# Optimization experiments

Hardware: AMD Instinct MI355X
Metric: run time of the kernel (lower is better)

Reference implementation:

```python
import jax, jax.numpy as jnp
import numpy as np

N_NODES = 20000
N_EDGES = 640000
HIDDEN = 128


def setup_inputs() -> dict:
    key = jax.random.key(0)
    k1, k2, k3, k4 = jax.random.split(key, 4)
    scale = 1.0 / np.sqrt(HIDDEN)
    features = jax.random.normal(k1, (N_NODES, HIDDEN), dtype=jnp.float32)
    edge_index = jax.random.randint(k2, (2, N_EDGES), 0, N_NODES, dtype=jnp.int64)
    W_l = jax.random.normal(k3, (HIDDEN, HIDDEN), dtype=jnp.float32) * scale
    b_l = jnp.zeros((HIDDEN,), dtype=jnp.float32)
    W_r = jax.random.normal(k4, (HIDDEN, HIDDEN), dtype=jnp.float32) * scale
    return {"features": features, "edge_index": edge_index, "W_l": W_l, "b_l": b_l, "W_r": W_r}


def reference(features, edge_index, W_l, b_l, W_r):
    # PyG SAGEConv with mean aggregation:
    #   out_i = lin_l(mean_{j : (j->i) in E} x_j) + lin_r(x_i)
    # edge_index[0] = source nodes, edge_index[1] = target nodes.
    n = features.shape[0]
    src = edge_index[0]
    dst = edge_index[1]
    msg = features[src]  # [E, d] gather
    summed = jax.ops.segment_sum(msg, dst, num_segments=n)  # [N, d] scatter-add
    cnt = jax.ops.segment_sum(jnp.ones(src.shape[0], dtype=features.dtype), dst, num_segments=n)
    agg = summed / jnp.maximum(cnt, 1.0)[:, None]  # mean; isolated nodes -> 0
    return agg @ W_l.T + b_l + features @ W_r.T
```

## Files before the change

kernel.cpp:

```cpp
#include <hip/hip_runtime.h>

#define N_NODES 20000
#define N_EDGES 640000
#define HIDDEN  128
#define CAP     96
#define DEG_PAD 16

typedef unsigned short bf16_t;
typedef __attribute__((ext_vector_type(8))) short short8;
typedef __attribute__((ext_vector_type(8))) unsigned short ushort8_t;
typedef __attribute__((ext_vector_type(4))) float floatx4;

__device__ __forceinline__ bf16_t f2bf(float f) {
    union { float f; unsigned int i; } v; v.f = f;
    unsigned int x = v.i + 0x7FFFu + ((v.i >> 16) & 1u);
    return (bf16_t)(x >> 16);
}
__device__ __forceinline__ float bflo(unsigned u) {
    union { unsigned i; float f; } v; v.i = u << 16; return v.f;
}
__device__ __forceinline__ float bfhi(unsigned u) {
    union { unsigned i; float f; } v; v.i = u & 0xFFFF0000u; return v.f;
}

__global__ __launch_bounds__(256) void prep_fill_kernel(
        const float* __restrict__ feat,
        const float* __restrict__ Wl,
        const float* __restrict__ Wr,
        const int* __restrict__ eidx,
        bf16_t* __restrict__ feat_bf,
        bf16_t* __restrict__ Bp,
        int* __restrict__ deg,
        unsigned short* __restrict__ bucket) {
    int t = blockIdx.x * 256 + threadIdx.x;
    float4 v = ((const float4*)feat)[t];
    ushort4 o = { f2bf(v.x), f2bf(v.y), f2bf(v.z), f2bf(v.w) };
    ((ushort4*)feat_bf)[t] = o;
    int src = eidx[t];
    int dst = eidx[N_EDGES + t];
    int pos = atomicAdd(&deg[dst * DEG_PAD], 1);
    if (pos < CAP) bucket[dst * CAP + pos] = (unsigned short)src;
    if (t < 2 * HIDDEN * HIDDEN) {
        int j    = t & 7;
        int lane = (t >> 3) & 63;
        int nt   = (t >> 9) & 7;
        int kt   = t >> 12;
        int n = nt * 16 + (lane & 15);
        int k = kt * 32 + (lane >> 4) * 8 + j;
        float w = (k < HIDDEN) ? Wl[n * HIDDEN + k] : Wr[n * HIDDEN + (k - HIDDEN)];
        Bp[t] = f2bf(w);
    }
}

__global__ __launch_bounds__(256) void agg_kernel(
        const bf16_t* __restrict__ feat_bf,
        const int* __restrict__ deg,
        const unsigned short* __restrict__ bucket,
        bf16_t* __restrict__ agg) {
    int wid  = (blockIdx.x * 256 + threadIdx.x) >> 6;
    int lane = threadIdx.x & 63;
    if (wid >= N_NODES) return;
    int d_true = deg[wid * DEG_PAD];
    int d = min(d_true, CAP);
    const unsigned short* row = bucket + wid * CAP;
    const unsigned* y = (const unsigned*)feat_bf;
    float ax0=0,ay0=0, ax1=0,ay1=0, ax2=0,ay2=0, ax3=0,ay3=0;
    int i = 0;
    for (; i + 16 <= d; i += 16) {
        ushort8_t s0 = *(const ushort8_t*)(row + i);
        ushort8_t s1 = *(const ushort8_t*)(row + i + 8);
        unsigned u0 = y[(int)s0[0] * 64 + lane];
        unsigned u1 = y[(int)s0[1] * 64 + lane];
        unsigned u2 = y[(int)s0[2] * 64 + lane];
        unsigned u3 = y[(int)s0[3] * 64 + lane];
        unsigned u4 = y[(int)s0[4] * 64 + lane];
        unsigned u5 = y[(int)s0[5] * 64 + lane];
        unsigned u6 = y[(int)s0[6] * 64 + lane];
        unsigned u7 = y[(int)s0[7] * 64 + lane];
        unsigned w0 = y[(int)s1[0] * 64 + lane];
        unsigned w1 = y[(int)s1[1] * 64 + lane];
        unsigned w2 = y[(int)s1[2] * 64 + lane];
        unsigned w3 = y[(int)s1[3] * 64 + lane];
        unsigned w4 = y[(int)s1[4] * 64 + lane];
        unsigned w5 = y[(int)s1[5] * 64 + lane];
        unsigned w6 = y[(int)s1[6] * 64 + lane];
        unsigned w7 = y[(int)s1[7] * 64 + lane];
        ax0 += bflo(u0); ay0 += bfhi(u0);
        ax1 += bflo(u1); ay1 += bfhi(u1);
        ax2 += bflo(u2); ay2 += bfhi(u2);
        ax3 += bflo(u3); ay3 += bfhi(u3);
        ax0 += bflo(u4); ay0 += bfhi(u4);
        ax1 += bflo(u5); ay1 += bfhi(u5);
        ax2 += bflo(u6); ay2 += bfhi(u6);
        ax3 += bflo(u7); ay3 += bfhi(u7);
        ax0 += bflo(w0); ay0 += bfhi(w0);
        ax1 += bflo(w1); ay1 += bfhi(w1);
        ax2 += bflo(w2); ay2 += bfhi(w2);
        ax3 += bflo(w3); ay3 += bfhi(w3);
        ax0 += bflo(w4); ay0 += bfhi(w4);
        ax1 += bflo(w5); ay1 += bfhi(w5);
        ax2 += bflo(w6); ay2 += bfhi(w6);
        ax3 += bflo(w7); ay3 += bfhi(w7);
    }
    for (; i + 8 <= d; i += 8) {
        ushort8_t s = *(const ushort8_t*)(row + i);
        unsigned u0 = y[(int)s[0] * 64 + lane];
        unsigned u1 = y[(int)s[1] * 64 + lane];
        unsigned u2 = y[(int)s[2] * 64 + lane];
        unsigned u3 = y[(int)s[3] * 64 + lane];
        unsigned u4 = y[(int)s[4] * 64 + lane];
        unsigned u5 = y[(int)s[5] * 64 + lane];
        unsigned u6 = y[(int)s[6] * 64 + lane];
        unsigned u7 = y[(int)s[7] * 64 + lane];
        ax0 += bflo(u0); ay0 += bfhi(u0);
        ax1 += bflo(u1); ay1 += bfhi(u1);
        ax2 += bflo(u2); ay2 += bfhi(u2);
        ax3 += bflo(u3); ay3 += bfhi(u3);
        ax0 += bflo(u4); ay0 += bfhi(u4);
        ax1 += bflo(u5); ay1 += bfhi(u5);
        ax2 += bflo(u6); ay2 += bfhi(u6);
        ax3 += bflo(u7); ay3 += bfhi(u7);
    }
    for (; i < d; ++i) {
        unsigned u = y[(int)row[i] * 64 + lane];
        ax0 += bflo(u); ay0 += bfhi(u);
    }
    float inv = 1.0f / fmaxf((float)d_true, 1.0f);
    float sx = (ax0 + ax1 + ax2 + ax3) * inv;
    float sy = (ay0 + ay1 + ay2 + ay3) * inv;
    unsigned pk = (unsigned)f2bf(sx) | ((unsigned)f2bf(sy) << 16);
    ((unsigned*)agg)[wid * 64 + lane] = pk;
}

__global__ __launch_bounds__(256) void gemm_out_kernel(
        const bf16_t* __restrict__ agg,
        const bf16_t* __restrict__ feat_bf,
        const bf16_t* __restrict__ Bp,
        const float* __restrict__ bl,
        float* __restrict__ out) {
    int wid = blockIdx.x * 4 + (threadIdx.x >> 6);
    if (wid >= N_NODES / 16) return;
    int lane = threadIdx.x & 63;
    int m    = lane & 15;
    int quad = lane >> 4;
    int row0 = wid * 16;

    floatx4 acc[8];
    floatx4 zf = {0.f, 0.f, 0.f, 0.f};
#pragma unroll
    for (int nt = 0; nt < 8; ++nt) acc[nt] = zf;

    const short8* bp = (const short8*)Bp;
#pragma unroll
    for (int kt = 0; kt < 8; ++kt) {
        const bf16_t* abase = (kt < 4)
            ? (agg     + (size_t)(row0 + m) * HIDDEN + kt * 32 + quad * 8)
            : (feat_bf + (size_t)(row0 + m) * HIDDEN + (kt - 4) * 32 + quad * 8);
        short8 afrag = *(const short8*)abase;
#pragma unroll
        for (int nt = 0; nt < 8; ++nt) {
            short8 bfrag = bp[(kt * 8 + nt) * 64 + lane];
            acc[nt] = __builtin_amdgcn_mfma_f32_16x16x32_bf16(afrag, bfrag, acc[nt], 0, 0, 0);
        }
    }
    int col = lane & 15;
#pragma unroll
    for (int nt = 0; nt < 8; ++nt) {
        float b = bl[nt * 16 + col];
#pragma unroll
        for (int r = 0; r < 4; ++r) {
            int row = row0 + quad * 4 + r;
            out[(size_t)row * HIDDEN + nt * 16 + col] = acc[nt][r] + b;
        }
    }
}

extern "C" void kernel_launch(void* const* d_in, const int* in_sizes, int n_in,
                              void* d_out, int out_size, void* d_ws, size_t ws_size,
                              hipStream_t stream) {
    const float* feat = (const float*)d_in[0];
    const int*   eidx = (const int*)d_in[1];
    const float* Wl   = (const float*)d_in[2];
    const float* bl   = (const float*)d_in[3];
    const float* Wr   = (const float*)d_in[4];
    float* out = (float*)d_out;

    int*            deg     = (int*)d_ws;
    unsigned short* bucket  = (unsigned short*)(deg + N_NODES * DEG_PAD);
    bf16_t*         Bp      = (bf16_t*)(bucket + (size_t)N_NODES * CAP);
    bf16_t*         feat_bf = Bp + 2 * HIDDEN * HIDDEN;
    bf16_t*         agg     = feat_bf + (size_t)N_NODES * HIDDEN;

    hipMemsetAsync(deg, 0, (size_t)N_NODES * DEG_PAD * sizeof(int), stream);

    prep_fill_kernel<<<N_EDGES / 256, 256, 0, stream>>>(
        feat, Wl, Wr, eidx, feat_bf, Bp, deg, bucket);
    agg_kernel<<<(N_NODES * 64) / 256, 256, 0, stream>>>(feat_bf, deg, bucket, agg);
    gemm_out_kernel<<<(N_NODES / 16 + 3) / 4, 256, 0, stream>>>(agg, feat_bf, Bp, bl, out);
}
```

Measured before the change: 135.3 us.

## Fuse neighbor aggregation into GEMM kernel via shared-memory tile

Merges the aggregation and output GEMM kernels into one. Each 256-thread block now aggregates 16 nodes, with each wave handling 4 nodes in sequence, and writes the bf16 means into a padded LDS tile. The block then runs the MFMA GEMM, reading the aggregated half of the A operand from LDS. This removes one kernel launch and the global write and re-read of the agg buffer. In exchange, each wave processes 4 nodes serially, so there are fewer independent waves to hide gather latency, and the GEMM phase waits at a block barrier.

New measurement: 151.6 us. 12.0% more time.

```diff
diff --git a/kernel.cpp b/kernel.cpp
--- a/kernel.cpp
+++ b/kernel.cpp
@@ -5,6 +5,7 @@
 #define HIDDEN  128
 #define CAP     96
 #define DEG_PAD 16
+#define LDSP    136
 
 typedef unsigned short bf16_t;
 typedef __attribute__((ext_vector_type(8))) short short8;
@@ -52,99 +53,95 @@
     }
 }
 
-__global__ __launch_bounds__(256) void agg_kernel(
-        const bf16_t* __restrict__ feat_bf,
-        const int* __restrict__ deg,
-        const unsigned short* __restrict__ bucket,
-        bf16_t* __restrict__ agg) {
-    int wid  = (blockIdx.x * 256 + threadIdx.x) >> 6;
-    int lane = threadIdx.x & 63;
-    if (wid >= N_NODES) return;
-    int d_true = deg[wid * DEG_PAD];
-    int d = min(d_true, CAP);
-    const unsigned short* row = bucket + wid * CAP;
-    const unsigned* y = (const unsigned*)feat_bf;
-    float ax0=0,ay0=0, ax1=0,ay1=0, ax2=0,ay2=0, ax3=0,ay3=0;
-    int i = 0;
-    for (; i + 16 <= d; i += 16) {
-        ushort8_t s0 = *(const ushort8_t*)(row + i);
-        ushort8_t s1 = *(const ushort8_t*)(row + i + 8);
-        unsigned u0 = y[(int)s0[0] * 64 + lane];
-        unsigned u1 = y[(int)s0[1] * 64 + lane];
-        unsigned u2 = y[(int)s0[2] * 64 + lane];
-        unsigned u3 = y[(int)s0[3] * 64 + lane];
-        unsigned u4 = y[(int)s0[4] * 64 + lane];
-        unsigned u5 = y[(int)s0[5] * 64 + lane];
-        unsigned u6 = y[(int)s0[6] * 64 + lane];
-        unsigned u7 = y[(int)s0[7] * 64 + lane];
-        unsigned w0 = y[(int)s1[0] * 64 + lane];
-        unsigned w1 = y[(int)s1[1] * 64 + lane];
-        unsigned w2 = y[(int)s1[2] * 64 + lane];
-        unsigned w3 = y[(int)s1[3] * 64 + lane];
-        unsigned w4 = y[(int)s1[4] * 64 + lane];
-        unsigned w5 = y[(int)s1[5] * 64 + lane];
-        unsigned w6 = y[(int)s1[6] * 64 + lane];
-        unsigned w7 = y[(int)s1[7] * 64 + lane];
-        ax0 += bflo(u0); ay0 += bfhi(u0);
-        ax1 += bflo(u1); ay1 += bfhi(u1);
-        ax2 += bflo(u2); ay2 += bfhi(u2);
-        ax3 += bflo(u3); ay3 += bfhi(u3);
-        ax0 += bflo(u4); ay0 += bfhi(u4);
-        ax1 += bflo(u5); ay1 += bfhi(u5);
-        ax2 += bflo(u6); ay2 += bfhi(u6);
-        ax3 += bflo(u7); ay3 += bfhi(u7);
-        ax0 += bflo(w0); ay0 += bfhi(w0);
-        ax1 += bflo(w1); ay1 += bfhi(w1);
-        ax2 += bflo(w2); ay2 += bfhi(w2);
-        ax3 += bflo(w3); ay3 += bfhi(w3);
-        ax0 += bflo(w4); ay0 += bfhi(w4);
-        ax1 += bflo(w5); ay1 += bfhi(w5);
-        ax2 += bflo(w6); ay2 += bfhi(w6);
-        ax3 += bflo(w7); ay3 += bfhi(w7);
-    }
-    for (; i + 8 <= d; i += 8) {
-        ushort8_t s = *(const ushort8_t*)(row + i);
-        unsigned u0 = y[(int)s[0] * 64 + lane];
-        unsigned u1 = y[(int)s[1] * 64 + lane];
-        unsigned u2 = y[(int)s[2] * 64 + lane];
-        unsigned u3 = y[(int)s[3] * 64 + lane];
-        unsigned u4 = y[(int)s[4] * 64 + lane];
-        unsigned u5 = y[(int)s[5] * 64 + lane];
-        unsigned u6 = y[(int)s[6] * 64 + lane];
-        unsigned u7 = y[(int)s[7] * 64 + lane];
-        ax0 += bflo(u0); ay0 += bfhi(u0);
-        ax1 += bflo(u1); ay1 += bfhi(u1);
-        ax2 += bflo(u2); ay2 += bfhi(u2);
-        ax3 += bflo(u3); ay3 += bfhi(u3);
-        ax0 += bflo(u4); ay0 += bfhi(u4);
-        ax1 += bflo(u5); ay1 += bfhi(u5);
-        ax2 += bflo(u6); ay2 += bfhi(u6);
-        ax3 += bflo(u7); ay3 += bfhi(u7);
-    }
-    for (; i < d; ++i) {
-        unsigned u = y[(int)row[i] * 64 + lane];
-        ax0 += bflo(u); ay0 += bfhi(u);
-    }
-    float inv = 1.0f / fmaxf((float)d_true, 1.0f);
-    float sx = (ax0 + ax1 + ax2 + ax3) * inv;
-    float sy = (ay0 + ay1 + ay2 + ay3) * inv;
-    unsigned pk = (unsigned)f2bf(sx) | ((unsigned)f2bf(sy) << 16);
-    ((unsigned*)agg)[wid * 64 + lane] = pk;
-}
-
-__global__ __launch_bounds__(256) void gemm_out_kernel(
-        const bf16_t* __restrict__ agg,
+__global__ __launch_bounds__(256) void agg_gemm_kernel(
         const bf16_t* __restrict__ feat_bf,
         const bf16_t* __restrict__ Bp,
         const float* __restrict__ bl,
+        const int* __restrict__ deg,
+        const unsigned short* __restrict__ bucket,
         float* __restrict__ out) {
-    int wid = blockIdx.x * 4 + (threadIdx.x >> 6);
-    if (wid >= N_NODES / 16) return;
+    __shared__ bf16_t aggT[16 * LDSP];
+    int wave = threadIdx.x >> 6;
     int lane = threadIdx.x & 63;
+    int row0 = blockIdx.x * 16;
+    const unsigned* y = (const unsigned*)feat_bf;
+
+    for (int nn = 0; nn < 4; ++nn) {
+        int node = row0 + wave * 4 + nn;
+        int d_true = deg[node * DEG_PAD];
+        int d = min(d_true, CAP);
+        const unsigned short* row = bucket + (size_t)node * CAP;
+        float ax0=0,ay0=0, ax1=0,ay1=0, ax2=0,ay2=0, ax3=0,ay3=0;
+        int i = 0;
+        for (; i + 16 <= d; i += 16) {
+            ushort8_t s0 = *(const ushort8_t*)(row + i);
+            ushort8_t s1 = *(const ushort8_t*)(row + i + 8);
+            unsigned u0 = y[(int)s0[0] * 64 + lane];
+            unsigned u1 = y[(int)s0[1] * 64 + lane];
+            unsigned u2 = y[(int)s0[2] * 64 + lane];
+            unsigned u3 = y[(int)s0[3] * 64 + lane];
+            unsigned u4 = y[(int)s0[4] * 64 + lane];
+            unsigned u5 = y[(int)s0[5] * 64 + lane];
+            unsigned u6 = y[(int)s0[6] * 64 + lane];
+            unsigned u7 = y[(int)s0[7] * 64 + lane];
+            unsigned w0 = y[(int)s1[0] * 64 + lane];
+            unsigned w1 = y[(int)s1[1] * 64 + lane];
+            unsigned w2 = y[(int)s1[2] * 64 + lane];
+            unsigned w3 = y[(int)s1[3] * 64 + lane];
+            unsigned w4 = y[(int)s1[4] * 64 + lane];
+            unsigned w5 = y[(int)s1[5] * 64 + lane];
+            unsigned w6 = y[(int)s1[6] * 64 + lane];
+            unsigned w7 = y[(int)s1[7] * 64 + lane];
+            ax0 += bflo(u0); ay0 += bfhi(u0);
+            ax1 += bflo(u1); ay1 += bfhi(u1);
+            ax2 += bflo(u2); ay2 += bfhi(u2);
+            ax3 += bflo(u3); ay3 += bfhi(u3);
+            ax0 += bflo(u4); ay0 += bfhi(u4);
+            ax1 += bflo(u5); ay1 += bfhi(u5);
+            ax2 += bflo(u6); ay2 += bfhi(u6);
+            ax3 += bflo(u7); ay3 += bfhi(u7);
+            ax0 += bflo(w0); ay0 += bfhi(w0);
+            ax1 += bflo(w1); ay1 += bfhi(w1);
+            ax2 += bflo(w2); ay2 += bfhi(w2);
+            ax3 += bflo(w3); ay3 += bfhi(w3);
+            ax0 += bflo(w4); ay0 += bfhi(w4);
+            ax1 += bflo(w5); ay1 += bfhi(w5);
+            ax2 += bflo(w6); ay2 += bfhi(w6);
+            ax3 += bflo(w7); ay3 += bfhi(w7);
+        }
+        for (; i + 8 <= d; i += 8) {
+            ushort8_t s = *(const ushort8_t*)(row + i);
+            unsigned u0 = y[(int)s[0] * 64 + lane];
+            unsigned u1 = y[(int)s[1] * 64 + lane];
+            unsigned u2 = y[(int)s[2] * 64 + lane];
+            unsigned u3 = y[(int)s[3] * 64 + lane];
+            unsigned u4 = y[(int)s[4] * 64 + lane];
+            unsigned u5 = y[(int)s[5] * 64 + lane];
+            unsigned u6 = y[(int)s[6] * 64 + lane];
+            unsigned u7 = y[(int)s[7] * 64 + lane];
+            ax0 += bflo(u0); ay0 += bfhi(u0);
+            ax1 += bflo(u1); ay1 += bfhi(u1);
+            ax2 += bflo(u2); ay2 += bfhi(u2);
+            ax3 += bflo(u3); ay3 += bfhi(u3);
+            ax0 += bflo(u4); ay0 += bfhi(u4);
+            ax1 += bflo(u5); ay1 += bfhi(u5);
+            ax2 += bflo(u6); ay2 += bfhi(u6);
+            ax3 += bflo(u7); ay3 += bfhi(u7);
+        }
+        for (; i < d; ++i) {
+            unsigned u = y[(int)row[i] * 64 + lane];
+            ax0 += bflo(u); ay0 += bfhi(u);
+        }
+        float inv = 1.0f / fmaxf((float)d_true, 1.0f);
+        float sx = (ax0 + ax1 + ax2 + ax3) * inv;
+        float sy = (ay0 + ay1 + ay2 + ay3) * inv;
+        unsigned pk = (unsigned)f2bf(sx) | ((unsigned)f2bf(sy) << 16);
+        ((unsigned*)&aggT[(wave * 4 + nn) * LDSP])[lane] = pk;
+    }
+    __syncthreads();
+
     int m    = lane & 15;
     int quad = lane >> 4;
-    int row0 = wid * 16;
-
     floatx4 acc[8];
     floatx4 zf = {0.f, 0.f, 0.f, 0.f};
 #pragma unroll
@@ -153,10 +150,13 @@
     const short8* bp = (const short8*)Bp;
 #pragma unroll
     for (int kt = 0; kt < 8; ++kt) {
-        const bf16_t* abase = (kt < 4)
-            ? (agg     + (size_t)(row0 + m) * HIDDEN + kt * 32 + quad * 8)
-            : (feat_bf + (size_t)(row0 + m) * HIDDEN + (kt - 4) * 32 + quad * 8);
-        short8 afrag = *(const short8*)abase;
+        short8 afrag;
+        if (kt < 4) {
+            afrag = *(const short8*)(&aggT[m * LDSP + kt * 32 + quad * 8]);
+        } else {
+            afrag = *(const short8*)(feat_bf + (size_t)(row0 + m) * HIDDEN
+                                     + (kt - 4) * 32 + quad * 8);
+        }
 #pragma unroll
         for (int nt = 0; nt < 8; ++nt) {
             short8 bfrag = bp[(kt * 8 + nt) * 64 + lane];
@@ -189,12 +189,11 @@
     unsigned short* bucket  = (unsigned short*)(deg + N_NODES * DEG_PAD);
     bf16_t*         Bp      = (bf16_t*)(bucket + (size_t)N_NODES * CAP);
     bf16_t*         feat_bf = Bp + 2 * HIDDEN * HIDDEN;
-    bf16_t*         agg     = feat_bf + (size_t)N_NODES * HIDDEN;
 
     hipMemsetAsync(deg, 0, (size_t)N_NODES * DEG_PAD * sizeof(int), stream);
 
     prep_fill_kernel<<<N_EDGES / 256, 256, 0, stream>>>(
         feat, Wl, Wr, eidx, feat_bf, Bp, deg, bucket);
-    agg_kernel<<<(N_NODES * 64) / 256, 256, 0, stream>>>(feat_bf, deg, bucket, agg);
-    gemm_out_kernel<<<(N_NODES / 16 + 3) / 4, 256, 0, stream>>>(agg, feat_bf, Bp, bl, out);
+    agg_gemm_kernel<<<N_NODES / 16, 256, 0, stream>>>(
+        feat_bf, Bp, bl, deg, bucket, out);
 }
```

## Split aggregation into two column-half passes with split-edge wavefronts

Applied to the files above, without the earlier changes.

The gather-aggregate kernel becomes two launches, each covering half of the 128 feature columns. Within a wavefront, the two 32-lane halves process alternate edges and their partial sums are combined with a cross-lane shuffle. The aim is to shrink the live gather working set per pass (half the feature table, about 2.5 MB) so it fits better in L2, and to double the number of edges in flight per wave. The cost is an extra kernel launch, rereading the bucket and degree arrays twice, and narrower 128-byte row accesses per gather.

After: 142.6 us. 1.05x slower.

```diff
diff --git a/kernel.cpp b/kernel.cpp
--- a/kernel.cpp
+++ b/kernel.cpp
@@ -52,39 +52,61 @@
     }
 }
 
-__global__ __launch_bounds__(256) void agg_kernel(
+__global__ __launch_bounds__(256) void agg_half_kernel(
         const bf16_t* __restrict__ feat_bf,
         const int* __restrict__ deg,
         const unsigned short* __restrict__ bucket,
-        bf16_t* __restrict__ agg) {
+        bf16_t* __restrict__ agg,
+        int half) {
     int wid  = (blockIdx.x * 256 + threadIdx.x) >> 6;
     int lane = threadIdx.x & 63;
     if (wid >= N_NODES) return;
+    int c   = lane & 31;
+    int sub = lane >> 5;
     int d_true = deg[wid * DEG_PAD];
     int d = min(d_true, CAP);
-    const unsigned short* row = bucket + wid * CAP;
-    const unsigned* y = (const unsigned*)feat_bf;
+    const unsigned short* row = bucket + (size_t)wid * CAP;
+    const unsigned* yh = (const unsigned*)feat_bf + half * 32 + c;
+
     float ax0=0,ay0=0, ax1=0,ay1=0, ax2=0,ay2=0, ax3=0,ay3=0;
-    int i = 0;
-    for (; i + 16 <= d; i += 16) {
-        ushort8_t s0 = *(const ushort8_t*)(row + i);
-        ushort8_t s1 = *(const ushort8_t*)(row + i + 8);
-        unsigned u0 = y[(int)s0[0] * 64 + lane];
-        unsigned u1 = y[(int)s0[1] * 64 + lane];
-        unsigned u2 = y[(int)s0[2] * 64 + lane];
-        unsigned u3 = y[(int)s0[3] * 64 + lane];
-        unsigned u4 = y[(int)s0[4] * 64 + lane];
-        unsigned u5 = y[(int)s0[5] * 64 + lane];
-        unsigned u6 = y[(int)s0[6] * 64 + lane];
-        unsigned u7 = y[(int)s0[7] * 64 + lane];
-        unsigned w0 = y[(int)s1[0] * 64 + lane];
-        unsigned w1 = y[(int)s1[1] * 64 + lane];
-        unsigned w2 = y[(int)s1[2] * 64 + lane];
-        unsigned w3 = y[(int)s1[3] * 64 + lane];
-        unsigned w4 = y[(int)s1[4] * 64 + lane];
-        unsigned w5 = y[(int)s1[5] * 64 + lane];
-        unsigned w6 = y[(int)s1[6] * 64 + lane];
-        unsigned w7 = y[(int)s1[7] * 64 + lane];
+    int k = 0;
+    for (; k + 32 <= d; k += 32) {
+        ushort8_t s0 = *(const ushort8_t*)(row + k);
+        ushort8_t s1 = *(const ushort8_t*)(row + k + 8);
+        ushort8_t s2 = *(const ushort8_t*)(row + k + 16);
+        ushort8_t s3 = *(const ushort8_t*)(row + k + 24);
+        int a0 = sub ? (int)s0[1] : (int)s0[0];
+        int a1 = sub ? (int)s0[3] : (int)s0[2];
+        int a2 = sub ? (int)s0[5] : (int)s0[4];
+        int a3 = sub ? (int)s0[7] : (int)s0[6];
+        int a4 = sub ? (int)s1[1] : (int)s1[0];
+        int a5 = sub ? (int)s1[3] : (int)s1[2];
+        int a6 = sub ? (int)s1[5] : (int)s1[4];
+        int a7 = sub ? (int)s1[7] : (int)s1[6];
+        int b0 = sub ? (int)s2[1] : (int)s2[0];
+        int b1 = sub ? (int)s2[3] : (int)s2[2];
+        int b2 = sub ? (int)s2[5] : (int)s2[4];
+        int b3 = sub ? (int)s2[7] : (int)s2[6];
+        int b4 = sub ? (int)s3[1] : (int)s3[0];
+        int b5 = sub ? (int)s3[3] : (int)s3[2];
+        int b6 = sub ? (int)s3[5] : (int)s3[4];
+        int b7 = sub ? (int)s3[7] : (int)s3[6];
+        unsigned u0 = yh[a0 * 64];
+        unsigned u1 = yh[a1 * 64];
+        unsigned u2 = yh[a2 * 64];
+        unsigned u3 = yh[a3 * 64];
+        unsigned u4 = yh[a4 * 64];
+        unsigned u5 = yh[a5 * 64];
+        unsigned u6 = yh[a6 * 64];
+        unsigned u7 = yh[a7 * 64];
+        unsigned v0 = yh[b0 * 64];
+        unsigned v1 = yh[b1 * 64];
+        unsigned v2 = yh[b2 * 64];
+        unsigned v3 = yh[b3 * 64];
+        unsigned v4 = yh[b4 * 64];
+        unsigned v5 = yh[b5 * 64];
+        unsigned v6 = yh[b6 * 64];
+        unsigned v7 = yh[b7 * 64];
         ax0 += bflo(u0); ay0 += bfhi(u0);
         ax1 += bflo(u1); ay1 += bfhi(u1);
         ax2 += bflo(u2); ay2 += bfhi(u2);
@@ -93,25 +115,34 @@
         ax1 += bflo(u5); ay1 += bfhi(u5);
         ax2 += bflo(u6); ay2 += bfhi(u6);
         ax3 += bflo(u7); ay3 += bfhi(u7);
-        ax0 += bflo(w0); ay0 += bfhi(w0);
-        ax1 += bflo(w1); ay1 += bfhi(w1);
-        ax2 += bflo(w2); ay2 += bfhi(w2);
-        ax3 += bflo(w3); ay3 += bfhi(w3);
-        ax0 += bflo(w4); ay0 += bfhi(w4);
-        ax1 += bflo(w5); ay1 += bfhi(w5);
-        ax2 += bflo(w6); ay2 += bfhi(w6);
-        ax3 += bflo(w7); ay3 += bfhi(w7);
-    }
-    for (; i + 8 <= d; i += 8) {
-        ushort8_t s = *(const ushort8_t*)(row + i);
-        unsigned u0 = y[(int)s[0] * 64 + lane];
-        unsigned u1 = y[(int)s[1] * 64 + lane];
-        unsigned u2 = y[(int)s[2] * 64 + lane];
-        unsigned u3 = y[(int)s[3] * 64 + lane];
-        unsigned u4 = y[(int)s[4] * 64 + lane];
-        unsigned u5 = y[(int)s[5] * 64 + lane];
-        unsigned u6 = y[(int)s[6] * 64 + lane];
-        unsigned u7 = y[(int)s[7] * 64 + lane];
+        ax0 += bflo(v0); ay0 += bfhi(v0);
+        ax1 += bflo(v1); ay1 += bfhi(v1);
+        ax2 += bflo(v2); ay2 += bfhi(v2);
+        ax3 += bflo(v3); ay3 += bfhi(v3);
+        ax0 += bflo(v4); ay0 += bfhi(v4);
+        ax1 += bflo(v5); ay1 += bfhi(v5);
+        ax2 += bflo(v6); ay2 += bfhi(v6);
+        ax3 += bflo(v7); ay3 += bfhi(v7);
+    }
+    for (; k + 16 <= d; k += 16) {
+        ushort8_t s0 = *(const ushort8_t*)(row + k);
+        ushort8_t s1 = *(const ushort8_t*)(row + k + 8);
+        int a0 = sub ? (int)s0[1] : (int)s0[0];
+        int a1 = sub ? (int)s0[3] : (int)s0[2];
+        int a2 = sub ? (int)s0[5] : (int)s0[4];
+        int a3 = sub ? (int)s0[7] : (int)s0[6];
+        int a4 = sub ? (int)s1[1] : (int)s1[0];
+        int a5 = sub ? (int)s1[3] : (int)s1[2];
+        int a6 = sub ? (int)s1[5] : (int)s1[4];
+        int a7 = sub ? (int)s1[7] : (int)s1[6];
+        unsigned u0 = yh[a0 * 64];
+        unsigned u1 = yh[a1 * 64];
+        unsigned u2 = yh[a2 * 64];
+        unsigned u3 = yh[a3 * 64];
+        unsigned u4 = yh[a4 * 64];
+        unsigned u5 = yh[a5 * 64];
+        unsigned u6 = yh[a6 * 64];
+        unsigned u7 = yh[a7 * 64];
         ax0 += bflo(u0); ay0 += bfhi(u0);
         ax1 += bflo(u1); ay1 += bfhi(u1);
         ax2 += bflo(u2); ay2 += bfhi(u2);
@@ -121,15 +152,26 @@
         ax2 += bflo(u6); ay2 += bfhi(u6);
         ax3 += bflo(u7); ay3 += bfhi(u7);
     }
-    for (; i < d; ++i) {
-        unsigned u = y[(int)row[i] * 64 + lane];
+    for (; k + 2 <= d; k += 2) {
+        int ia = (int)row[k + sub];
+        unsigned u = yh[ia * 64];
         ax0 += bflo(u); ay0 += bfhi(u);
     }
-    float inv = 1.0f / fmaxf((float)d_true, 1.0f);
-    float sx = (ax0 + ax1 + ax2 + ax3) * inv;
-    float sy = (ay0 + ay1 + ay2 + ay3) * inv;
-    unsigned pk = (unsigned)f2bf(sx) | ((unsigned)f2bf(sy) << 16);
-    ((unsigned*)agg)[wid * 64 + lane] = pk;
+    if (k < d) {
+        int ia = (int)row[k];
+        unsigned u = yh[ia * 64];
+        u = sub ? 0u : u;
+        ax0 += bflo(u); ay0 += bfhi(u);
+    }
+    float sx = (ax0 + ax1) + (ax2 + ax3);
+    float sy = (ay0 + ay1) + (ay2 + ay3);
+    sx += __shfl_xor(sx, 32);
+    sy += __shfl_xor(sy, 32);
+    if (sub == 0) {
+        float inv = 1.0f / fmaxf((float)d_true, 1.0f);
+        unsigned pk = (unsigned)f2bf(sx * inv) | ((unsigned)f2bf(sy * inv) << 16);
+        ((unsigned*)agg)[wid * 64 + half * 32 + c] = pk;
+    }
 }
 
 __global__ __launch_bounds__(256) void gemm_out_kernel(
@@ -195,6 +237,10 @@
 
     prep_fill_kernel<<<N_EDGES / 256, 256, 0, stream>>>(
         feat, Wl, Wr, eidx, feat_bf, Bp, deg, bucket);
-    agg_kernel<<<(N_NODES * 64) / 256, 256, 0, stream>>>(feat_bf, deg, bucket, agg);
-    gemm_out_kernel<<<(N_NODES / 16 + 3) / 4, 256, 0, stream>>>(agg, feat_bf, Bp, bl, out);
-}
+    agg_half_kernel<<<(N_NODES * 64) / 256, 256, 0, stream>>>(
+        feat_bf, deg, bucket, agg, 0);
+    agg_half_kernel<<<(N_NODES * 64) / 256, 256, 0, stream>>>(
+        feat_bf, deg, bucket, agg, 1);
+    gemm_out_kernel<<<(N_NODES / 16 + 3) / 4, 256, 0, stream>>>(
+        agg, feat_bf, Bp, bl, out);
+}
```
